# Optimization experiments

Hardware: AMD Instinct MI355X
Metric: run time of the kernel (lower is better)

## Reference

```python
import jax, jax.numpy as jnp
import numpy as np

B, C, H, W = 4, 256, 48, 48
NH = 4                 # num_heads
HD = C // NH           # head_dim = 64
KD = HD // 2           # key_dim = 32 (attn_ratio=0.5)
QKV_C = C + 2 * KD * NH  # 512
FF = 2 * C             # 512
EPS = 1e-3             # ultralytics BatchNorm2d eps


def _bn(x, g, b, m, v):
    # eval-mode BatchNorm2d over channel dim 1 of NCHW
    s = g / jnp.sqrt(v + EPS)
    return x * s[:, None, None] + (b - m * s)[:, None, None]


def _conv1x1(x, w):
    # w: [out_c, in_c]
    return jnp.einsum('bchw,oc->bohw', x, w)


def _dwconv3x3(x, w):
    # depthwise 3x3, padding 1; w: [C, 1, 3, 3]
    return jax.lax.conv_general_dilated(
        x, w, (1, 1), [(1, 1), (1, 1)],
        dimension_numbers=('NCHW', 'OIHW', 'NCHW'),
        feature_group_count=C)


def setup_inputs() -> dict:
    key = jax.random.key(0)
    ks = jax.random.split(key, 32)
    d = {}
    d['x'] = jax.random.normal(ks[0], (B, C, H, W), dtype=jnp.float32)

    def bn_params(i, ch):
        g = 0.5 + jax.random.uniform(ks[i], (ch,), dtype=jnp.float32)
        b = 0.1 * jax.random.normal(ks[i + 1], (ch,), dtype=jnp.float32)
        m = 0.1 * jax.random.normal(ks[i + 2], (ch,), dtype=jnp.float32)
        v = 0.5 + jax.random.uniform(ks[i + 3], (ch,), dtype=jnp.float32)
        return g, b, m, v

    d['qkv_w'] = 0.05 * jax.random.normal(ks[1], (QKV_C, C), dtype=jnp.float32)
    d['qkv_g'], d['qkv_b'], d['qkv_m'], d['qkv_v'] = bn_params(2, QKV_C)
    d['pe_w'] = 0.1 * jax.random.normal(ks[6], (C, 1, 3, 3), dtype=jnp.float32)
    d['pe_g'], d['pe_b'], d['pe_m'], d['pe_v'] = bn_params(7, C)
    d['proj_w'] = 0.05 * jax.random.normal(ks[11], (C, C), dtype=jnp.float32)
    d['proj_g'], d['proj_b'], d['proj_m'], d['proj_v'] = bn_params(12, C)
    d['f1_w'] = 0.05 * jax.random.normal(ks[16], (FF, C), dtype=jnp.float32)
    d['f1_g'], d['f1_b'], d['f1_m'], d['f1_v'] = bn_params(17, FF)
    d['f2_w'] = 0.05 * jax.random.normal(ks[21], (C, FF), dtype=jnp.float32)
    d['f2_g'], d['f2_b'], d['f2_m'], d['f2_v'] = bn_params(22, C)
    return d


def reference(x, qkv_w, qkv_g, qkv_b, qkv_m, qkv_v,
              pe_w, pe_g, pe_b, pe_m, pe_v,
              proj_w, proj_g, proj_b, proj_m, proj_v,
              f1_w, f1_g, f1_b, f1_m, f1_v,
              f2_w, f2_g, f2_b, f2_m, f2_v):
    b, c, h, w = x.shape
    n = h * w
    # --- Attention ---
    qkv = _bn(_conv1x1(x, qkv_w), qkv_g, qkv_b, qkv_m, qkv_v)
    qkv = qkv.reshape(b, NH, 2 * KD + HD, n)
    q = qkv[:, :, :KD]            # [b, nh, kd, n]
    k = qkv[:, :, KD:2 * KD]      # [b, nh, kd, n]
    v = qkv[:, :, 2 * KD:]        # [b, nh, hd, n]
    attn = jnp.einsum('bhkn,bhkm->bhnm', q, k) * (KD ** -0.5)
    attn = jax.nn.softmax(attn, axis=-1)
    o = jnp.einsum('bhdm,bhnm->bhdn', v, attn).reshape(b, c, h, w)
    pe = _bn(_dwconv3x3(v.reshape(b, c, h, w), pe_w), pe_g, pe_b, pe_m, pe_v)
    attn_out = _bn(_conv1x1(o + pe, proj_w), proj_g, proj_b, proj_m, proj_v)
    x = x + attn_out  # shortcut
    # --- FFN ---
    f = _conv1x1(x, f1_w)
    f = _bn(f, f1_g, f1_b, f1_m, f1_v)
    f = f * jax.nn.sigmoid(f)  # SiLU
    f = _bn(_conv1x1(f, f2_w), f2_g, f2_b, f2_m, f2_v)
    return x + f  # shortcut
```

## Files before the change

### kernel.cpp

```cpp
#include <hip/hip_runtime.h>
#include <math.h>

#define Bb   4
#define Cc   256
#define Hh   48
#define Ww   48
#define NNp  2304
#define Rr   9216
#define NHd  4
#define QKVC 512
#define EPSf 1e-3f

typedef unsigned int   u32;
typedef unsigned short u16;
typedef __attribute__((ext_vector_type(8))) __bf16 bf16x8;
typedef __attribute__((ext_vector_type(4))) float  f32x4;

#if __has_builtin(__builtin_amdgcn_exp2f)
#define EXP2F(x) __builtin_amdgcn_exp2f(x)
#else
#define EXP2F(x) __expf((x) * 0.6931471805599453f)
#endif

__device__ __forceinline__ u16 f2bf(float f) {
    u32 u = __float_as_uint(f);
    u = (u + 0x7fffu + ((u >> 16) & 1u)) >> 16;
    return (u16)u;
}
__device__ __forceinline__ float bf2f(u16 h) {
    return __uint_as_float((u32)h << 16);
}
__device__ __forceinline__ u32 pk2bf(float a, float b) {
    union { __bf16 h; u16 u; } ua, ub;
    ua.h = (__bf16)a; ub.h = (__bf16)b;
    return (u32)ua.u | ((u32)ub.u << 16);
}
__device__ __forceinline__ void gload16(const void* gsrc, void* ldst) {
    __builtin_amdgcn_global_load_lds(
        (const __attribute__((address_space(1))) u32*)gsrc,
        (__attribute__((address_space(3))) u32*)ldst, 16, 0, 0);
}

__global__ __launch_bounds__(64)
void prep_all(const float* __restrict__ W0, const float* __restrict__ g0, const float* __restrict__ b0, const float* __restrict__ m0, const float* __restrict__ v0, u16* __restrict__ Wb0, float* __restrict__ bi0,
              const float* __restrict__ W1, const float* __restrict__ g1, const float* __restrict__ b1, const float* __restrict__ m1, const float* __restrict__ v1, u16* __restrict__ Wb1, float* __restrict__ bi1,
              const float* __restrict__ W2, const float* __restrict__ g2, const float* __restrict__ b2, const float* __restrict__ m2, const float* __restrict__ v2, u16* __restrict__ Wb2, float* __restrict__ bi2,
              const float* __restrict__ W3, const float* __restrict__ g3, const float* __restrict__ b3, const float* __restrict__ m3, const float* __restrict__ v3, u16* __restrict__ Wb3, float* __restrict__ bi3)
{
    const int bid = blockIdx.x;
    const float *W, *gp, *bp, *mp, *vp;
    u16* Wb; float* bias;
    int K = 256, oc;
    float c = 1.f;
    if (bid < 512) {
        oc = bid; W = W0; gp = g0; bp = b0; mp = m0; vp = v0; Wb = Wb0; bias = bi0;
        if ((oc & 127) < 32) c = 0.17677669529663687f * 1.4426950408889634f;
    } else if (bid < 768) {
        oc = bid - 512; W = W1; gp = g1; bp = b1; mp = m1; vp = v1; Wb = Wb1; bias = bi1;
    } else if (bid < 1280) {
        oc = bid - 768; W = W2; gp = g2; bp = b2; mp = m2; vp = v2; Wb = Wb2; bias = bi2;
    } else {
        oc = bid - 1280; W = W3; gp = g3; bp = b3; mp = m3; vp = v3; Wb = Wb3; bias = bi3;
        K = 512;
    }
    const int lane = threadIdx.x;
    const float s = gp[oc] * rsqrtf(vp[oc] + EPSf);
    if (lane == 0) bias[oc] = (bp[oc] - mp[oc] * s) * c;
    const float sc = s * c;
    for (int k0 = lane * 4; k0 < K; k0 += 256) {
        const float4 w = *(const float4*)(W + (size_t)oc * K + k0);
        u32 lo = (u32)f2bf(w.x * sc) | ((u32)f2bf(w.y * sc) << 16);
        u32 hi = (u32)f2bf(w.z * sc) | ((u32)f2bf(w.w * sc) << 16);
        *(uint2*)(Wb + (size_t)oc * K + k0) = make_uint2(lo, hi);
    }
}

__global__ __launch_bounds__(256)
void cvt_x(const float* __restrict__ x, u16* __restrict__ Xt)
{
    const int b = blockIdx.z, c0 = blockIdx.y * 64, n0 = blockIdx.x * 64;
    __shared__ float tile[64][65];
    const int tid = threadIdx.x;
    {
        const int n = tid & 63, cl = tid >> 6;
        #pragma unroll
        for (int cc = 0; cc < 16; ++cc) {
            const int c = cc * 4 + cl;
            tile[c][n] = x[((size_t)b * Cc + c0 + c) * NNp + n0 + n];
        }
    }
    __syncthreads();
    {
        const int n = tid >> 2, q = tid & 3;
        #pragma unroll
        for (int j = 0; j < 2; ++j) {
            const int ch = q * 2 + j, c = ch * 8;
            u32 w[4];
            #pragma unroll
            for (int e = 0; e < 4; ++e)
                w[e] = (u32)f2bf(tile[c + 2*e][n]) | ((u32)f2bf(tile[c + 2*e + 1][n]) << 16);
            *(uint4*)(Xt + ((size_t)b * NNp + n0 + n) * Cc + c0 + c)
                = make_uint4(w[0], w[1], w[2], w[3]);
        }
    }
}

template<int BN_, int FN_, int MODE>
__global__ __launch_bounds__(256)
void gemm_mfma(const u16* __restrict__ A, const u16* __restrict__ Bx,
               const float* __restrict__ bias, const float* __restrict__ resid,
               float* __restrict__ Yf, u16* __restrict__ Yt, int M, int K)
{
    constexpr int WN = FN_ * 16;
    const int r0 = blockIdx.x * BN_;
    const int m0 = blockIdx.y * 128;
    const int tid = threadIdx.x;
    const int lane = tid & 63, wid = tid >> 6;
    const int g = lane >> 4, i16 = lane & 15;
    const int wr = wid >> 1, wc = wid & 1;

    __shared__ __align__(16) u16 Al[2][4][128][8];
    __shared__ __align__(16) u16 Bl[2][4][BN_][8];

    f32x4 acc[4][FN_];
    #pragma unroll
    for (int i = 0; i < 4; ++i)
        #pragma unroll
        for (int j = 0; j < FN_; ++j) acc[i][j] = (f32x4){0.f, 0.f, 0.f, 0.f};

    #pragma unroll
    for (int ii = 0; ii < 2; ++ii) {
        const int ci = ii * 256 + tid;
        gload16(A + (size_t)(m0 + (ci & 127)) * K + (ci >> 7) * 8,
                (u16*)&Al[0][0][0][0] + (size_t)ci * 8);
    }
    if (BN_ == 128) {
        #pragma unroll
        for (int ii = 0; ii < 2; ++ii) {
            const int ci = ii * 256 + tid;
            gload16(Bx + (size_t)(r0 + (ci & 127)) * K + (ci >> 7) * 8,
                    (u16*)&Bl[0][0][0][0] + (size_t)ci * 8);
        }
    } else {
        gload16(Bx + (size_t)(r0 + (tid & 63)) * K + (tid >> 6) * 8,
                (u16*)&Bl[0][0][0][0] + (size_t)tid * 8);
    }
    __syncthreads();

    int buf = 0;
    for (int k0 = 0; k0 < K; k0 += 32) {
        if (k0 + 32 < K) {
            const int kn = k0 + 32;
            #pragma unroll
            for (int ii = 0; ii < 2; ++ii) {
                const int ci = ii * 256 + tid;
                gload16(A + (size_t)(m0 + (ci & 127)) * K + kn + (ci >> 7) * 8,
                        (u16*)&Al[buf ^ 1][0][0][0] + (size_t)ci * 8);
            }
            if (BN_ == 128) {
                #pragma unroll
                for (int ii = 0; ii < 2; ++ii) {
                    const int ci = ii * 256 + tid;
                    gload16(Bx + (size_t)(r0 + (ci & 127)) * K + kn + (ci >> 7) * 8,
                            (u16*)&Bl[buf ^ 1][0][0][0] + (size_t)ci * 8);
                }
            } else {
                gload16(Bx + (size_t)(r0 + (tid & 63)) * K + kn + (tid >> 6) * 8,
                        (u16*)&Bl[buf ^ 1][0][0][0] + (size_t)tid * 8);
            }
        }
        bf16x8 af[4], bf[FN_];
        #pragma unroll
        for (int ao = 0; ao < 4; ++ao)
            af[ao] = *(const bf16x8*)&Al[buf][g][wr * 64 + ao * 16 + i16][0];
        #pragma unroll
        for (int bo = 0; bo < FN_; ++bo)
            bf[bo] = *(const bf16x8*)&Bl[buf][g][wc * WN + bo * 16 + i16][0];
        __builtin_amdgcn_s_setprio(1);
        #pragma unroll
        for (int ao = 0; ao < 4; ++ao)
            #pragma unroll
            for (int bo = 0; bo < FN_; ++bo)
                acc[ao][bo] = __builtin_amdgcn_mfma_f32_16x16x32_bf16(
                    af[ao], bf[bo], acc[ao][bo], 0, 0, 0);
        __builtin_amdgcn_s_setprio(0);
        __syncthreads();
        buf ^= 1;
    }

    const int b  = r0 / NNp;
    const int nb = r0 - b * NNp;
    #pragma unroll
    for (int ao = 0; ao < 4; ++ao) {
        const int oc0 = m0 + wr * 64 + ao * 16 + g * 4;
        const float4 t4 = *(const float4*)(bias + oc0);
        #pragma unroll
        for (int bo = 0; bo < FN_; ++bo) {
            const int nloc = wc * WN + bo * 16 + i16;
            float y[4];
            y[0] = acc[ao][bo][0] + t4.x;  y[1] = acc[ao][bo][1] + t4.y;
            y[2] = acc[ao][bo][2] + t4.z;  y[3] = acc[ao][bo][3] + t4.w;
            if (MODE == 1 || MODE == 3) {
                const int n = nb + nloc;
                const size_t base = ((size_t)b * M + oc0) * NNp + n;
                #pragma unroll
                for (int r = 0; r < 4; ++r) {
                    y[r] += resid[base + (size_t)r * NNp];
                    Yf[base + (size_t)r * NNp] = y[r];
                }
            }
            if (MODE == 2) {
                #pragma unroll
                for (int r = 0; r < 4; ++r) y[r] = y[r] / (1.f + __expf(-y[r]));
            }
            if (MODE != 3) {
                const size_t rG = (size_t)(r0 + nloc);
                u32 lo = (u32)f2bf(y[0]) | ((u32)f2bf(y[1]) << 16);
                u32 hi = (u32)f2bf(y[2]) | ((u32)f2bf(y[3]) << 16);
                *(uint2*)(Yt + rG * M + oc0) = make_uint2(lo, hi);
            }
        }
    }
}

__global__ __launch_bounds__(256)
void repack_v(const u16* __restrict__ Yt, u16* __restrict__ Vb)
{
    const int m0 = blockIdx.x * 64;
    const int h = blockIdx.y, b = blockIdx.z;
    const int bh = b * NHd + h;
    __shared__ u16 vt[64][72];
    const int tid = threadIdx.x;
    #pragma unroll
    for (int ii = 0; ii < 2; ++ii) {
        const int mm = ii * 32 + (tid >> 3);
        const int ch = tid & 7;
        *(uint4*)&vt[mm][ch * 8] =
            *(const uint4*)(Yt + ((size_t)b * NNp + m0 + mm) * QKVC + h * 128 + 64 + ch * 8);
    }
    __syncthreads();
    const int d = tid >> 2, mq = tid & 3;
    #pragma unroll
    for (int j = 0; j < 2; ++j) {
        const int mc = mq * 2 + j;
        u32 w[4];
        #pragma unroll
        for (int e = 0; e < 4; ++e)
            w[e] = (u32)vt[mc * 8 + 2*e][d] | ((u32)vt[mc * 8 + 2*e + 1][d] << 16);
        *(uint4*)(Vb + ((size_t)bh * 64 + d) * NNp + m0 + mc * 8)
            = make_uint4(w[0], w[1], w[2], w[3]);
    }
}

__global__ __launch_bounds__(128)
void attn_mfma(const u16* __restrict__ Yt, const u16* __restrict__ Vb,
               u16* __restrict__ Ot)
{
    __shared__ __align__(16) u16 Klds[2][4][64][8];
    __shared__ __align__(16) u16 Vlds[2][64][8][8];
    __shared__ __align__(16) u32 Plds[2][16][36];

    const int tid  = threadIdx.x;
    const int wid  = tid >> 6;
    const int lane = tid & 63;
    const int g    = lane >> 4;
    const int i16  = lane & 15;

    const int wg  = blockIdx.x;
    const int swz = (wg & 7) * 144 + (wg >> 3);
    const int xq  = swz % 72;
    const int bh  = swz / 72;
    const int h   = bh & 3, b = bh >> 2;

    const size_t bG = (size_t)b * NNp;
    const u16* Vg = Vb + (size_t)bh * 64 * NNp;

    const int nq = xq * 32 + wid * 16 + i16;
    const bf16x8 qfrag = *(const bf16x8*)(Yt + (bG + nq) * QKVC + h * 128 + g * 8);

    bf16x8 ones;
    { uint4 ov = make_uint4(0x3f803f80u, 0x3f803f80u, 0x3f803f80u, 0x3f803f80u);
      ones = *(bf16x8*)&ov; }

    const f32x4 zero = {0.f, 0.f, 0.f, 0.f};
    f32x4 oacc[4];
    f32x4 lacc = zero;
    #pragma unroll
    for (int d = 0; d < 4; ++d) oacc[d] = zero;
    float m_run = -1e30f;

    #pragma unroll
    for (int ii = 0; ii < 2; ++ii) {
        const int ci = ii * 128 + tid;
        gload16(Yt + (bG + (ci & 63)) * QKVC + h * 128 + 32 + (ci >> 6) * 8,
                (u16*)&Klds[0][0][0][0] + (size_t)ci * 8);
    }
    #pragma unroll
    for (int ii = 0; ii < 4; ++ii) {
        const int idx = ii * 128 + tid;
        const int d = idx >> 3, cp = idx & 7;
        gload16(Vg + (size_t)d * NNp + (cp ^ (d & 7)) * 8,
                (u16*)&Vlds[0][0][0][0] + (size_t)idx * 8);
    }
    __syncthreads();

    int cur = 0;
    for (int t = 0; t < 36; ++t) {
        if (t < 35) {
            const int m0 = (t + 1) * 64;
            #pragma unroll
            for (int ii = 0; ii < 2; ++ii) {
                const int ci = ii * 128 + tid;
                gload16(Yt + (bG + m0 + (ci & 63)) * QKVC + h * 128 + 32 + (ci >> 6) * 8,
                        (u16*)&Klds[cur ^ 1][0][0][0] + (size_t)ci * 8);
            }
            #pragma unroll
            for (int ii = 0; ii < 4; ++ii) {
                const int idx = ii * 128 + tid;
                const int d = idx >> 3, cp = idx & 7;
                gload16(Vg + (size_t)d * NNp + m0 + (cp ^ (d & 7)) * 8,
                        (u16*)&Vlds[cur ^ 1][0][0][0] + (size_t)idx * 8);
            }
        }

        f32x4 sac[4];
        __builtin_amdgcn_s_setprio(1);
        #pragma unroll
        for (int j = 0; j < 4; ++j) {
            const bf16x8 kf = *(const bf16x8*)&Klds[cur][g][16 * j + i16][0];
            sac[j] = __builtin_amdgcn_mfma_f32_16x16x32_bf16(kf, qfrag, zero, 0, 0, 0);
        }
        __builtin_amdgcn_s_setprio(0);

        float pm = sac[0][0];
        #pragma unroll
        for (int j = 0; j < 4; ++j)
            #pragma unroll
            for (int r = 0; r < 4; ++r) pm = fmaxf(pm, sac[j][r]);
        pm = fmaxf(pm, __shfl_xor(pm, 16));
        pm = fmaxf(pm, __shfl_xor(pm, 32));

        if (!__all(pm <= m_run + 8.f)) {
            const float mn = fmaxf(m_run, pm);
            const float fc = EXP2F(m_run - mn);
            m_run = mn;
            lacc[0] *= fc; lacc[1] *= fc; lacc[2] *= fc; lacc[3] *= fc;
            #pragma unroll
            for (int d = 0; d < 4; ++d) {
                oacc[d][0] *= fc; oacc[d][1] *= fc;
                oacc[d][2] *= fc; oacc[d][3] *= fc;
            }
        }

        {
            u32* prow = &Plds[wid][i16][0];
            #pragma unroll
            for (int j = 0; j < 4; ++j) {
                const float p0 = EXP2F(sac[j][0] - m_run);
                const float p1 = EXP2F(sac[j][1] - m_run);
                const float p2 = EXP2F(sac[j][2] - m_run);
                const float p3 = EXP2F(sac[j][3] - m_run);
                *(uint2*)&prow[8 * j + 2 * g] = make_uint2(pk2bf(p0, p1), pk2bf(p2, p3));
            }
        }

        const int d7 = i16 & 7;
        __builtin_amdgcn_s_setprio(1);
        #pragma unroll
        for (int s = 0; s < 2; ++s) {
            const bf16x8 pf = *(const bf16x8*)&Plds[wid][i16][16 * s + 4 * g];
            lacc = __builtin_amdgcn_mfma_f32_16x16x32_bf16(ones, pf, lacc, 0, 0, 0);
            #pragma unroll
            for (int db = 0; db < 4; ++db) {
                const bf16x8 vf = *(const bf16x8*)&Vlds[cur][db * 16 + i16][(4 * s + g) ^ d7][0];
                oacc[db] = __builtin_amdgcn_mfma_f32_16x16x32_bf16(vf, pf, oacc[db], 0, 0, 0);
            }
        }
        __builtin_amdgcn_s_setprio(0);

        __syncthreads();
        cur ^= 1;
    }

    const float linv = 1.f / lacc[0];
    u16* ob = Ot + (bG + nq) * Cc + h * 64;
    #pragma unroll
    for (int db = 0; db < 4; ++db) {
        u32 lo = pk2bf(oacc[db][0] * linv, oacc[db][1] * linv);
        u32 hi = pk2bf(oacc[db][2] * linv, oacc[db][3] * linv);
        *(uint2*)(ob + db * 16 + g * 4) = make_uint2(lo, hi);
    }
}

__global__ __launch_bounds__(256)
void pe_bn(const u16* __restrict__ Yt, const float* __restrict__ pw,
           const float* __restrict__ gg, const float* __restrict__ bb,
           const float* __restrict__ mm, const float* __restrict__ vv,
           u16* __restrict__ Ot)
{
    const int tid = threadIdx.x;
    const int h = blockIdx.y, b = blockIdx.z;
    const int p = blockIdx.x * 32 + (tid >> 3);
    const int ch = tid & 7;
    const int c0 = h * 64 + ch * 8;
    const int yy = p / Ww, xx = p - yy * Ww;

    float acc[8];
    #pragma unroll
    for (int j = 0; j < 8; ++j) acc[j] = 0.f;

    #pragma unroll
    for (int dy = -1; dy <= 1; ++dy) {
        const int Y = yy + dy;
        if (Y < 0 || Y >= Hh) continue;
        #pragma unroll
        for (int dx = -1; dx <= 1; ++dx) {
            const int X = xx + dx;
            if (X < 0 || X >= Ww) continue;
            const uint4 raw = *(const uint4*)(Yt +
                ((size_t)b * NNp + Y * Ww + X) * QKVC + h * 128 + 64 + ch * 8);
            const u32* rw = (const u32*)&raw;
            #pragma unroll
            for (int j = 0; j < 8; ++j) {
                const u16 hv = (u16)(rw[j >> 1] >> (16 * (j & 1)));
                acc[j] += pw[(size_t)(c0 + j) * 9 + (dy + 1) * 3 + (dx + 1)] * bf2f(hv);
            }
        }
    }

    u16* dst = Ot + ((size_t)b * NNp + p) * Cc + c0;
    uint4 old = *(uint4*)dst;
    u32* ow = (u32*)&old;
    u32 res[4];
    #pragma unroll
    for (int e = 0; e < 4; ++e) {
        u16 r0, r1;
        {
            const int j = 2 * e;
            const float s = gg[c0 + j] * rsqrtf(vv[c0 + j] + EPSf);
            const float t = bb[c0 + j] - mm[c0 + j] * s;
            r0 = f2bf(bf2f((u16)(ow[e] & 0xffff)) + acc[j] * s + t);
        }
        {
            const int j = 2 * e + 1;
            const float s = gg[c0 + j] * rsqrtf(vv[c0 + j] + EPSf);
            const float t = bb[c0 + j] - mm[c0 + j] * s;
            r1 = f2bf(bf2f((u16)(ow[e] >> 16)) + acc[j] * s + t);
        }
        res[e] = (u32)r0 | ((u32)r1 << 16);
    }
    *(uint4*)dst = make_uint4(res[0], res[1], res[2], res[3]);
}

extern "C" void kernel_launch(void* const* d_in, const int* in_sizes, int n_in,
                              void* d_out, int out_size, void* d_ws, size_t ws_size,
                              hipStream_t stream)
{
    const float* x      = (const float*)d_in[0];
    const float* qkv_w  = (const float*)d_in[1];
    const float* qkv_g  = (const float*)d_in[2];
    const float* qkv_b  = (const float*)d_in[3];
    const float* qkv_m  = (const float*)d_in[4];
    const float* qkv_v  = (const float*)d_in[5];
    const float* pe_w   = (const float*)d_in[6];
    const float* pe_g   = (const float*)d_in[7];
    const float* pe_b   = (const float*)d_in[8];
    const float* pe_m   = (const float*)d_in[9];
    const float* pe_v   = (const float*)d_in[10];
    const float* proj_w = (const float*)d_in[11];
    const float* proj_g = (const float*)d_in[12];
    const float* proj_b = (const float*)d_in[13];
    const float* proj_m = (const float*)d_in[14];
    const float* proj_v = (const float*)d_in[15];
    const float* f1_w   = (const float*)d_in[16];
    const float* f1_g   = (const float*)d_in[17];
    const float* f1_b   = (const float*)d_in[18];
    const float* f1_m   = (const float*)d_in[19];
    const float* f1_v   = (const float*)d_in[20];
    const float* f2_w   = (const float*)d_in[21];
    const float* f2_g   = (const float*)d_in[22];
    const float* f2_b   = (const float*)d_in[23];
    const float* f2_m   = (const float*)d_in[24];
    const float* f2_v   = (const float*)d_in[25];

    char* wsb = (char*)d_ws;
    u16*   Yt   = (u16*)(wsb);
    u16*   Xt   = (u16*)(wsb + 9437184);
    u16*   Vb   = (u16*)(wsb + 14155776);
    u16*   Ot   = (u16*)(wsb + 18874368);
    float* x1f  = (float*)(wsb + 23592960);
    u16*   Wq   = (u16*)(wsb + 33030144);
    u16*   Wp   = (u16*)(wsb + 33292288);
    u16*   W1   = (u16*)(wsb + 33423360);
    u16*   W2   = (u16*)(wsb + 33685504);
    float* biq  = (float*)(wsb + 33947648);
    float* bip  = (float*)(wsb + 33949696);
    float* bi1  = (float*)(wsb + 33950720);
    float* bi2  = (float*)(wsb + 33952768);
    u16*   Ft   = Yt;
    u16*   X1t  = Xt;
    float* out  = (float*)d_out;

    prep_all<<<dim3(1536), dim3(64), 0, stream>>>(
        qkv_w, qkv_g, qkv_b, qkv_m, qkv_v, Wq, biq,
        proj_w, proj_g, proj_b, proj_m, proj_v, Wp, bip,
        f1_w, f1_g, f1_b, f1_m, f1_v, W1, bi1,
        f2_w, f2_g, f2_b, f2_m, f2_v, W2, bi2);
    cvt_x<<<dim3(36, 4, 4), dim3(256), 0, stream>>>(x, Xt);

    gemm_mfma<128, 4, 0><<<dim3(72, 4), dim3(256), 0, stream>>>(
        Wq, Xt, biq, nullptr, nullptr, Yt, QKVC, 256);

    repack_v<<<dim3(36, 4, 4), dim3(256), 0, stream>>>(Yt, Vb);
    attn_mfma<<<dim3(1152), dim3(128), 0, stream>>>(Yt, Vb, Ot);
    pe_bn<<<dim3(72, 4, 4), dim3(256), 0, stream>>>(Yt, pe_w, pe_g, pe_b, pe_m, pe_v, Ot);

    gemm_mfma<64, 2, 1><<<dim3(144, 2), dim3(256), 0, stream>>>(
        Wp, Ot, bip, x, x1f, X1t, Cc, 256);

    gemm_mfma<128, 4, 2><<<dim3(72, 4), dim3(256), 0, stream>>>(
        W1, X1t, bi1, nullptr, nullptr, Ft, QKVC, 256);

    gemm_mfma<64, 2, 3><<<dim3(144, 2), dim3(256), 0, stream>>>(
        W2, Ft, bi2, x1f, out, nullptr, Cc, 512);
}
```

Before: 151.7 us.

## Split attention keys into two halves and merge partial softmax results

Splits each query tile's key range across two workgroups in flash-decoding style. Each workgroup writes unnormalized partial outputs plus its running max and sum, and a new merge kernel combines the two halves. V fragments are now loaded straight from global memory into registers instead of being staged through LDS. The intent is more parallelism and occupancy for the attention kernel. The cost is an extra kernel launch, the partial-output round trip through memory, and bf16 rounding of the unnormalized partial outputs.

Measured after the change: 201.2 us. +32.6%, slower.

```diff
diff --git a/kernel.cpp b/kernel.cpp
--- a/kernel.cpp
+++ b/kernel.cpp
@@ -252,12 +252,11 @@
     }
 }
 
-__global__ __launch_bounds__(128)
+__global__ __launch_bounds__(128, 4)
 void attn_mfma(const u16* __restrict__ Yt, const u16* __restrict__ Vb,
-               u16* __restrict__ Ot)
+               u16* __restrict__ PartO, float* __restrict__ Pml)
 {
     __shared__ __align__(16) u16 Klds[2][4][64][8];
-    __shared__ __align__(16) u16 Vlds[2][64][8][8];
     __shared__ __align__(16) u32 Plds[2][16][36];
 
     const int tid  = threadIdx.x;
@@ -267,9 +266,11 @@
     const int i16  = lane & 15;
 
     const int wg  = blockIdx.x;
-    const int swz = (wg & 7) * 144 + (wg >> 3);
-    const int xq  = swz % 72;
-    const int bh  = swz / 72;
+    const int idx = (wg & 7) * 288 + (wg >> 3);
+    const int kh  = idx & 1;
+    const int qt  = idx >> 1;
+    const int xq  = qt % 72;
+    const int bh  = qt / 72;
     const int h   = bh & 3, b = bh >> 2;
 
     const size_t bG = (size_t)b * NNp;
@@ -289,37 +290,35 @@
     for (int d = 0; d < 4; ++d) oacc[d] = zero;
     float m_run = -1e30f;
 
+    const int t0 = kh * 18;
+
     #pragma unroll
     for (int ii = 0; ii < 2; ++ii) {
         const int ci = ii * 128 + tid;
-        gload16(Yt + (bG + (ci & 63)) * QKVC + h * 128 + 32 + (ci >> 6) * 8,
+        gload16(Yt + (bG + t0 * 64 + (ci & 63)) * QKVC + h * 128 + 32 + (ci >> 6) * 8,
                 (u16*)&Klds[0][0][0][0] + (size_t)ci * 8);
     }
-    #pragma unroll
-    for (int ii = 0; ii < 4; ++ii) {
-        const int idx = ii * 128 + tid;
-        const int d = idx >> 3, cp = idx & 7;
-        gload16(Vg + (size_t)d * NNp + (cp ^ (d & 7)) * 8,
-                (u16*)&Vlds[0][0][0][0] + (size_t)idx * 8);
-    }
     __syncthreads();
 
     int cur = 0;
-    for (int t = 0; t < 36; ++t) {
-        if (t < 35) {
-            const int m0 = (t + 1) * 64;
+    for (int t = 0; t < 18; ++t) {
+        const int m0k = (t0 + t) * 64;
+
+        bf16x8 vf[2][4];
+        #pragma unroll
+        for (int s = 0; s < 2; ++s)
+            #pragma unroll
+            for (int db = 0; db < 4; ++db)
+                vf[s][db] = *(const bf16x8*)(Vg + (size_t)(db * 16 + i16) * NNp
+                                             + m0k + (4 * s + g) * 8);
+
+        if (t < 17) {
+            const int mn = m0k + 64;
             #pragma unroll
             for (int ii = 0; ii < 2; ++ii) {
                 const int ci = ii * 128 + tid;
-                gload16(Yt + (bG + m0 + (ci & 63)) * QKVC + h * 128 + 32 + (ci >> 6) * 8,
+                gload16(Yt + (bG + mn + (ci & 63)) * QKVC + h * 128 + 32 + (ci >> 6) * 8,
                         (u16*)&Klds[cur ^ 1][0][0][0] + (size_t)ci * 8);
-            }
-            #pragma unroll
-            for (int ii = 0; ii < 4; ++ii) {
-                const int idx = ii * 128 + tid;
-                const int d = idx >> 3, cp = idx & 7;
-                gload16(Vg + (size_t)d * NNp + m0 + (cp ^ (d & 7)) * 8,
-                        (u16*)&Vlds[cur ^ 1][0][0][0] + (size_t)idx * 8);
             }
         }
 
@@ -364,17 +363,15 @@
             }
         }
 
-        const int d7 = i16 & 7;
         __builtin_amdgcn_s_setprio(1);
         #pragma unroll
         for (int s = 0; s < 2; ++s) {
             const bf16x8 pf = *(const bf16x8*)&Plds[wid][i16][16 * s + 4 * g];
             lacc = __builtin_amdgcn_mfma_f32_16x16x32_bf16(ones, pf, lacc, 0, 0, 0);
             #pragma unroll
-            for (int db = 0; db < 4; ++db) {
-                const bf16x8 vf = *(const bf16x8*)&Vlds[cur][db * 16 + i16][(4 * s + g) ^ d7][0];
-                oacc[db] = __builtin_amdgcn_mfma_f32_16x16x32_bf16(vf, pf, oacc[db], 0, 0, 0);
-            }
+            for (int db = 0; db < 4; ++db)
+                oacc[db] = __builtin_amdgcn_mfma_f32_16x16x32_bf16(
+                    vf[s][db], pf, oacc[db], 0, 0, 0);
         }
         __builtin_amdgcn_s_setprio(0);
 
@@ -382,14 +379,56 @@
         cur ^= 1;
     }
 
-    const float linv = 1.f / lacc[0];
-    u16* ob = Ot + (bG + nq) * Cc + h * 64;
+    const int qloc = wid * 16 + i16;
+    const int prow = (qt * 2 + kh) * 32 + qloc;
+    if (g == 0) {
+        Pml[(size_t)prow * 2 + 0] = m_run;
+        Pml[(size_t)prow * 2 + 1] = lacc[0];
+    }
+    u16* po = PartO + (size_t)prow * 64;
     #pragma unroll
     for (int db = 0; db < 4; ++db) {
-        u32 lo = pk2bf(oacc[db][0] * linv, oacc[db][1] * linv);
-        u32 hi = pk2bf(oacc[db][2] * linv, oacc[db][3] * linv);
-        *(uint2*)(ob + db * 16 + g * 4) = make_uint2(lo, hi);
-    }
+        u32 lo = pk2bf(oacc[db][0], oacc[db][1]);
+        u32 hi = pk2bf(oacc[db][2], oacc[db][3]);
+        *(uint2*)(po + db * 16 + g * 4) = make_uint2(lo, hi);
+    }
+}
+
+__global__ __launch_bounds__(256)
+void merge_attn(const u16* __restrict__ PartO, const float* __restrict__ Pml,
+                u16* __restrict__ Ot)
+{
+    const int gid = blockIdx.x * 256 + threadIdx.x;
+    const int row = gid >> 3;
+    const int ch  = gid & 7;
+    const int qt  = row >> 5;
+    const int q   = row & 31;
+    const int bh  = qt / 72;
+    const int xq  = qt - bh * 72;
+    const int h   = bh & 3, b = bh >> 2;
+
+    const int p0 = (qt * 2) * 32 + q;
+    const int p1 = p0 + 32;
+    const float2 ml0 = *(const float2*)(Pml + (size_t)p0 * 2);
+    const float2 ml1 = *(const float2*)(Pml + (size_t)p1 * 2);
+    const float m  = fmaxf(ml0.x, ml1.x);
+    const float fa = EXP2F(ml0.x - m);
+    const float fb = EXP2F(ml1.x - m);
+    const float inv = 1.f / (ml0.y * fa + ml1.y * fb);
+
+    const uint4 a4 = *(const uint4*)(PartO + (size_t)p0 * 64 + ch * 8);
+    const uint4 b4 = *(const uint4*)(PartO + (size_t)p1 * 64 + ch * 8);
+    const u32* aw = (const u32*)&a4;
+    const u32* bw = (const u32*)&b4;
+    u32 res[4];
+    #pragma unroll
+    for (int e = 0; e < 4; ++e) {
+        const float y0 = (bf2f((u16)(aw[e] & 0xffff)) * fa + bf2f((u16)(bw[e] & 0xffff)) * fb) * inv;
+        const float y1 = (bf2f((u16)(aw[e] >> 16))    * fa + bf2f((u16)(bw[e] >> 16))    * fb) * inv;
+        res[e] = pk2bf(y0, y1);
+    }
+    *(uint4*)(Ot + ((size_t)b * NNp + xq * 32 + q) * Cc + h * 64 + ch * 8)
+        = make_uint4(res[0], res[1], res[2], res[3]);
 }
 
 __global__ __launch_bounds__(256)
@@ -499,6 +538,8 @@
     float* bi2  = (float*)(wsb + 33952768);
     u16*   Ft   = Yt;
     u16*   X1t  = Xt;
+    float* Pml  = (float*)Xt;
+    u16*   PartO= (u16*)x1f;
     float* out  = (float*)d_out;
 
     prep_all<<<dim3(1536), dim3(64), 0, stream>>>(
@@ -512,7 +553,8 @@
         Wq, Xt, biq, nullptr, nullptr, Yt, QKVC, 256);
 
     repack_v<<<dim3(36, 4, 4), dim3(256), 0, stream>>>(Yt, Vb);
-    attn_mfma<<<dim3(1152), dim3(128), 0, stream>>>(Yt, Vb, Ot);
+    attn_mfma<<<dim3(2304), dim3(128), 0, stream>>>(Yt, Vb, PartO, Pml);
+    merge_attn<<<dim3(1152), dim3(256), 0, stream>>>(PartO, Pml, Ot);
     pe_bn<<<dim3(72, 4, 4), dim3(256), 0, stream>>>(Yt, pe_w, pe_g, pe_b, pe_m, pe_v, Ot);
 
     gemm_mfma<64, 2, 1><<<dim3(144, 2), dim3(256), 0, stream>>>(
```
